# Performance work log

Hardware: AMD Instinct MI355X
Metric: run time of the kernel (lower is better)

## Reference

```python
import jax, jax.numpy as jnp
import numpy as np

NC = 8          # num_classes
NA = 5          # num_anchors
NOOBJ = 1.0     # noobject_scale
OBJ = 10.0      # object_scale
COORD = 1.0     # coord_scale
CLASS = 1.0     # class_scale
THRESH = 0.6    # sil_thresh
ANCHORS = np.array([1.08, 1.19, 3.42, 4.41, 6.63, 11.38, 9.42, 5.11, 16.62, 10.52], np.float32)


def _iou_xywh(px, py, pw, pl, gx, gy, gw, gl):
    # IoU of center-format boxes (matches bbox_ious with x1y1x2y2=False)
    mx = jnp.minimum(px - pw * 0.5, gx - gw * 0.5)
    Mx = jnp.maximum(px + pw * 0.5, gx + gw * 0.5)
    my = jnp.minimum(py - pl * 0.5, gy - gl * 0.5)
    My = jnp.maximum(py + pl * 0.5, gy + gl * 0.5)
    cw = pw + gw - (Mx - mx)
    ch = pl + gl - (My - my)
    inter = jnp.where((cw > 0) & (ch > 0), cw * ch, 0.0)
    return inter / (pw * pl + gw * gl - inter)


def setup_inputs() -> dict:
    key = jax.random.key(0)
    k1, k2, k3 = jax.random.split(key, 3)
    nB, nT, nH, nW = 16, 50, 96, 96
    output = jax.random.normal(k1, (nB, NA * (7 + NC), nH, nW), jnp.float32)
    t = jax.random.uniform(k2, (nB, nT, 7), jnp.float32)
    cls_col = jax.random.randint(k3, (nB, nT, 1), 0, NC).astype(jnp.float32)
    geom = t[..., 1:5] * 0.9 + 0.05            # x,y,w,l in (0,1), nonzero
    euler = t[..., 5:7] * 2.0 - 1.0            # im,re in [-1,1]
    target = jnp.concatenate([cls_col, geom, euler], axis=-1)
    return {"output": output, "target": target, "anchors": jnp.asarray(ANCHORS)}


def reference(output, target, anchors):
    sg = jax.lax.stop_gradient
    nB, _, nH, nW = output.shape
    nA, nC = NA, NC
    N = nB * nA * nH * nW

    out = output.reshape(nB, nA, 7 + nC, nH, nW)
    x = jax.nn.sigmoid(out[:, :, 0])
    y = jax.nn.sigmoid(out[:, :, 1])
    w = out[:, :, 2]
    l = out[:, :, 3]
    im = out[:, :, 4]
    re = out[:, :, 5]
    conf = jax.nn.sigmoid(out[:, :, 6])
    # [nB*nA, nC, nH*nW].transpose(1,2) -> flat [N, nC]
    cls_prob = out[:, :, 7:].transpose(0, 1, 3, 4, 2).reshape(N, nC)

    # ---- predicted boxes (detached, as in the torch .data path) ----
    anc = sg(anchors)
    aw = anc[0::2]
    ah = anc[1::2]
    grid_x = jnp.arange(nW, dtype=jnp.float32)[None, None, None, :]
    grid_y = jnp.arange(nH, dtype=jnp.float32)[None, None, :, None]
    px = sg(x) + grid_x
    py = sg(y) + grid_y
    pw = jnp.exp(sg(w)) * aw[None, :, None, None]
    pl = jnp.exp(sg(l)) * ah[None, :, None, None]

    # ---- build_targets (vectorized) ----
    tgt = sg(target)
    nT = tgt.shape[1]
    # break-at-first-zero semantics of the original loop
    valid = jnp.cumprod((tgt[:, :, 1] != 0).astype(jnp.int32), axis=1).astype(bool)  # [nB,nT]
    gx = tgt[:, :, 1] * nW
    gy = tgt[:, :, 2] * nH
    gw = tgt[:, :, 3] * nW
    gl = tgt[:, :, 4] * nH

    # pairwise IoU pred-vs-GT: [nB, nT, nA, nH, nW]
    ious = _iou_xywh(px[:, None], py[:, None], pw[:, None], pl[:, None],
                     gx[:, :, None, None, None], gy[:, :, None, None, None],
                     gw[:, :, None, None, None], gl[:, :, None, None, None])
    ious = jnp.where(valid[:, :, None, None, None], ious, 0.0)
    max_iou = ious.max(axis=1)                              # [nB,nA,nH,nW]
    conf_mask = jnp.where(max_iou > THRESH, 0.0, NOOBJ)

    # best anchor per GT: IoU of (0,0,gw,gl) vs (0,0,aw,ah)
    inter = jnp.minimum(gw[..., None], aw) * jnp.minimum(gl[..., None], ah)
    anc_iou = inter / (gw[..., None] * gl[..., None] + aw * ah - inter)    # [nB,nT,nA]
    best_n = jnp.argmax(anc_iou, axis=-1)                   # first max, like strict '>' scan

    gi = jnp.clip(gx.astype(jnp.int32), 0, nW - 1)
    gj = jnp.clip(gy.astype(jnp.int32), 0, nH - 1)
    b_idx = jnp.arange(nB)[:, None]
    idx = ((b_idx * nA + best_n) * nH + gj) * nW + gi       # [nB,nT] flat cell index
    idx_safe = jnp.minimum(idx, N - 1)
    idx_sc = jnp.where(valid, idx, N).ravel()               # OOB -> dropped by scatter

    def scat(vals):
        return jnp.zeros(N, jnp.float32).at[idx_sc].set(vals.ravel(), mode='drop').reshape(nB, nA, nH, nW)

    coord_mask = scat(jnp.ones_like(gx))
    cls_mask_f = coord_mask.reshape(N)
    conf_mask = conf_mask.reshape(N).at[idx_sc].set(jnp.full(nB * nT, OBJ), mode='drop').reshape(nB, nA, nH, nW)

    tx = scat(gx - gi)
    ty = scat(gy - gj)
    tw = scat(jnp.log(gw / aw[best_n]))
    tl = scat(jnp.log(gl / ah[best_n]))
    tim = scat(tgt[:, :, 5])
    tre = scat(tgt[:, :, 6])
    tcls_f = scat(tgt[:, :, 0]).reshape(N)

    # IoU of each GT with the predicted box at its assigned cell
    pb = jnp.stack([px, py, pw, pl], axis=-1).reshape(N, 4)
    pbg = pb[idx_safe]                                      # [nB,nT,4]
    iou_t = _iou_xywh(pbg[..., 0], pbg[..., 1], pbg[..., 2], pbg[..., 3], gx, gy, gw, gl)
    tconf = scat(iou_t)

    nGT = valid.sum()
    nCorrect = (valid & (iou_t > 0.5)).sum()

    # ---- losses ----
    def mse(a, t, m):
        return jnp.sum((a * m - t * m) ** 2)

    loss_x = COORD * mse(x, tx, coord_mask)
    loss_y = COORD * mse(y, ty, coord_mask)
    loss_w = COORD * mse(w, tw, coord_mask)
    loss_l = COORD * mse(l, tl, coord_mask)
    loss_conf = mse(conf, tconf, conf_mask)
    loss_im = COORD * mse(im, tim, coord_mask)
    loss_re = COORD * mse(re, tre, coord_mask)

    logp = jax.nn.log_softmax(cls_prob, axis=-1)
    tcls_idx = tcls_f.astype(jnp.int32)
    ce = -jnp.take_along_axis(logp, tcls_idx[:, None], axis=1)[:, 0]
    loss_cls = CLASS * jnp.sum(ce * cls_mask_f)

    loss = loss_x + loss_y + loss_w + loss_l + loss_conf + loss_cls + loss_im + loss_re
    return loss, nCorrect, nGT
```

## Files before the change

kernel.cpp:

```cpp
#include <hip/hip_runtime.h>
#include <math.h>

namespace {

constexpr int kB = 16, kT = 50, kH = 96, kW = 96, kA = 5;
constexpr int kCH = 15;
constexpr int kPlane = kH * kW;
constexpr int kCellsPerBlk = 1024;
constexpr int kBlkPerPlane = kPlane / kCellsPerBlk;
constexpr int kNoobjBlocks = kB * kA * kBlkPerPlane;
constexpr int kReducerBlk = kB + kNoobjBlocks;
constexpr float kObjSq = 100.0f;


__device__ __forceinline__ void publish(unsigned long long* slot, float v) {
  unsigned lo = __float_as_uint(v);
  unsigned long long pk = ((unsigned long long)(~lo) << 32) | lo;
  atomicExch(slot, pk);
}

__device__ __forceinline__ float fast_sigmoid(float v) {
  return __builtin_amdgcn_rcpf(1.0f + __expf(-v));
}

__device__ __forceinline__ void make_rec(
    const float* __restrict__ tgt, const float* __restrict__ anc, int b,
    int lane, float4& r, float& c, int& vidx, bool& valid, float& gx,
    float& gy, float& gw, float& gl, int& bn, int& gi, int& gj, float& c0,
    float& e5, float& e6) {
  const float* tp = tgt + (b * kT + (lane < kT ? lane : 0)) * 7;
  c0 = tp[0];
  const float g1 = tp[1], g2 = tp[2], g3 = tp[3], g4 = tp[4];
  e5 = tp[5];
  e6 = tp[6];
  unsigned long long nzm = __ballot((lane < kT) && (g1 != 0.0f));
  valid = false;
  vidx = -1;
  bn = 0; gi = 0; gj = 0;
  gx = g1 * kW; gy = g2 * kH; gw = g3 * kW; gl = g4 * kH;
  r = make_float4(1e30f, -1e30f, 1e30f, -1e30f);
  c = 1e30f;
  if (lane < kT) {
    valid = ((~nzm) & ((1ull << (lane + 1)) - 1ull)) == 0ull;
    float best = -1.0f;
    for (int a = 0; a < kA; ++a) {
      float aw = anc[2 * a], ah = anc[2 * a + 1];
      float inter = fminf(gw, aw) * fminf(gl, ah);
      float iou = inter / (gw * gl + aw * ah - inter);
      if (iou > best) { best = iou; bn = a; }
    }
    gi = min(max((int)gx, 0), kW - 1);
    gj = min(max((int)gy, 0), kH - 1);
    int idx = ((b * kA + bn) * kH + gj) * kW + gi;
    vidx = valid ? idx : -1;
    if (valid) {
      r = make_float4(gx - gw * 0.5f, gx + gw * 0.5f, gy - gl * 0.5f,
                      gy + gl * 0.5f);
      c = 0.375f * (gw * gl);
    }
  }
}

__global__ __launch_bounds__(256) void fused_kernel(
    const float* __restrict__ out, const float* __restrict__ tgt,
    const float* __restrict__ anc, unsigned long long* __restrict__ ws,
    float* __restrict__ d_out) {
  __shared__ float s_red[4];

  const int blk = blockIdx.x;
  const int tid = threadIdx.x;

  if (blk == kReducerBlk) {
    float L = 0.0f, C = 0.0f, G = 0.0f;
    for (int s = tid; s < 768; s += 256) {
      unsigned long long v;
      for (;;) {
        v = atomicAdd(&ws[s], 0ULL);
        if ((unsigned)(v >> 32) == (unsigned)(~(unsigned)v)) break;
        __builtin_amdgcn_s_sleep(2);
      }
      float f = __uint_as_float((unsigned)v);
      if (s < 736) L += f;
      else if (s < 752) C += f;
      else G += f;
    }
    for (int off = 32; off > 0; off >>= 1) {
      L += __shfl_down(L, off, 64);
      C += __shfl_down(C, off, 64);
      G += __shfl_down(G, off, 64);
    }
    __shared__ float sr[12];
    const int wv = tid >> 6;
    if ((tid & 63) == 0) { sr[wv] = L; sr[4 + wv] = C; sr[8 + wv] = G; }
    __syncthreads();
    if (tid == 0) {
      d_out[0] = sr[0] + sr[1] + sr[2] + sr[3];
      d_out[1] = sr[4] + sr[5] + sr[6] + sr[7];
      d_out[2] = sr[8] + sr[9] + sr[10] + sr[11];
    }
    return;
  }

  if (blk < kB) {
    if (tid >= 64) return;
    const int b = blk, t = tid;
    float4 r; float c; int vidx; bool valid;
    float gx, gy, gw, gl, c0, e5, e6; int bn, gi, gj;
    make_rec(tgt, anc, b, t, r, c, vidx, valid, gx, gy, gw, gl, bn, gi, gj,
             c0, e5, e6);
    const int ngt = __popcll(__ballot(valid));

    float loss = 0.0f;
    int ncorr = 0;
    if (valid) {
      bool owner = true;
      for (int t2 = 0; t2 < kT; ++t2) {
        int v2 = __shfl(vidx, t2);
        owner &= !((t2 > t) && (v2 == vidx));
      }
      const float* p =
          out + ((size_t)(b * kA + bn) * kCH) * kPlane + gj * kW + gi;
      const float xr = p[0], yr = p[kPlane];
      const float wr = p[2 * kPlane], lr = p[3 * kPlane];
      const float aw = anc[2 * bn], ah = anc[2 * bn + 1];
      const float x = 1.0f / (1.0f + expf(-xr));
      const float y = 1.0f / (1.0f + expf(-yr));
      const float px = x + (float)gi, py = y + (float)gj;
      const float pw = expf(wr) * aw, pl = expf(lr) * ah;
      float mx = fminf(px - pw * 0.5f, gx - gw * 0.5f);
      float Mx = fmaxf(px + pw * 0.5f, gx + gw * 0.5f);
      float my = fminf(py - pl * 0.5f, gy - gl * 0.5f);
      float My = fmaxf(py + pl * 0.5f, gy + gl * 0.5f);
      float cw = pw + gw - (Mx - mx);
      float ch = pl + gl - (My - my);
      float inter = (cw > 0.0f && ch > 0.0f) ? cw * ch : 0.0f;
      float iou = inter / (pw * pl + gw * gl - inter);
      ncorr = (iou > 0.5f) ? 1 : 0;

      if (owner) {
        const float imv = p[4 * kPlane], rev = p[5 * kPlane];
        const float cr = p[6 * kPlane];
        float tx = gx - (float)gi, ty = gy - (float)gj;
        float tw = logf(gw / aw), tl = logf(gl / ah);
        float conf = 1.0f / (1.0f + expf(-cr));
        float dx = x - tx, dy = y - ty, dw = wr - tw, dl = lr - tl;
        float di = imv - e5, dr = rev - e6, dc = conf - iou;
        loss = dx * dx + dy * dy + dw * dw + dl * dl + di * di + dr * dr +
               kObjSq * dc * dc;
        const float cc0 = p[7 * kPlane],  cc1 = p[8 * kPlane];
        const float cc2 = p[9 * kPlane],  cc3 = p[10 * kPlane];
        const float cc4 = p[11 * kPlane], cc5 = p[12 * kPlane];
        const float cc6 = p[13 * kPlane], cc7 = p[14 * kPlane];
        float m = fmaxf(fmaxf(fmaxf(cc0, cc1), fmaxf(cc2, cc3)),
                        fmaxf(fmaxf(cc4, cc5), fmaxf(cc6, cc7)));
        float s = expf(cc0 - m) + expf(cc1 - m) + expf(cc2 - m) +
                  expf(cc3 - m) + expf(cc4 - m) + expf(cc5 - m) +
                  expf(cc6 - m) + expf(cc7 - m);
        float lse = m + logf(s);
        int ci = min(max((int)c0, 0), 7);
        float csel = cc0;
        csel = (ci == 1) ? cc1 : csel;
        csel = (ci == 2) ? cc2 : csel;
        csel = (ci == 3) ? cc3 : csel;
        csel = (ci == 4) ? cc4 : csel;
        csel = (ci == 5) ? cc5 : csel;
        csel = (ci == 6) ? cc6 : csel;
        csel = (ci == 7) ? cc7 : csel;
        loss += lse - csel;

        float pxf = fast_sigmoid(xr) + (float)gi;
        float pyf = fast_sigmoid(yr) + (float)gj;
        float pwf = __expf(wr) * aw, plf = __expf(lr) * ah;
        float px0 = pxf - pwf * 0.5f, px1 = pxf + pwf * 0.5f;
        float py0 = pyf - plf * 0.5f, py1 = pyf + plf * 0.5f;
        float pthr = 0.375f * (pwf * plf);
        float conff = fast_sigmoid(cr);
        float hh = -1e30f;
        for (int t2 = 0; t2 < kT; ++t2) {
          float x0 = __shfl(r.x, t2), x1 = __shfl(r.y, t2);
          float y0 = __shfl(r.z, t2), y1 = __shfl(r.w, t2);
          float cc = __shfl(c, t2);
          float cw2 = fminf(px1, x1) - fmaxf(px0, x0);
          float ch2 = fminf(py1, y1) - fmaxf(py0, y0);
          float a2 = fmaxf(cw2, 0.0f);
          hh = fmaxf(hh, __builtin_fmaf(a2, ch2, -cc));
        }
        if (!(hh > pthr)) loss -= conff * conff;
      }
    }
    for (int off = 32; off > 0; off >>= 1) {
      loss += __shfl_down(loss, off, 64);
      ncorr += __shfl_down(ncorr, off, 64);
    }
    if (t == 0) {
      publish(&ws[kNoobjBlocks + b], loss);
      publish(&ws[kNoobjBlocks + kB + b], (float)ncorr);
      publish(&ws[kNoobjBlocks + 2 * kB + b], (float)ngt);
    }
    return;
  }

  const int nb = blk - kB;
  const int plane = nb / kBlkPerPlane;
  const int b = plane / kA, a = plane % kA;
  const int base = (nb % kBlkPerPlane) * kCellsPerBlk;

  float4 r; float c; int vidx; bool valid;
  float gx, gy, gw, gl, c0, e5, e6; int bn, gi, gj;
  make_rec(tgt, anc, b, tid & 63, r, c, vidx, valid, gx, gy, gw, gl, bn, gi,
           gj, c0, e5, e6);

  const int cell0 = base + 4 * tid;
  const int j = cell0 / kW;
  const int i0 = cell0 - j * kW;

  const float* pb = out + ((size_t)plane * kCH) * kPlane + cell0;
  const float4 xv = *(const float4*)(pb);
  const float4 yv = *(const float4*)(pb + kPlane);
  const float4 wv = *(const float4*)(pb + 2 * kPlane);
  const float4 lv = *(const float4*)(pb + 3 * kPlane);
  const float4 cv = *(const float4*)(pb + 6 * kPlane);
  const float aw = anc[2 * a], ah = anc[2 * a + 1];

  const float xs[4] = {xv.x, xv.y, xv.z, xv.w};
  const float ys[4] = {yv.x, yv.y, yv.z, yv.w};
  const float wss[4] = {wv.x, wv.y, wv.z, wv.w};
  const float ls[4] = {lv.x, lv.y, lv.z, lv.w};
  const float crs[4] = {cv.x, cv.y, cv.z, cv.w};

  float px0[4], px1[4], py0[4], py1[4], pthr[4], conf[4], hh[4];
#pragma unroll
  for (int e = 0; e < 4; ++e) {
    float px = fast_sigmoid(xs[e]) + (float)(i0 + e);
    float py = fast_sigmoid(ys[e]) + (float)j;
    float pw = __expf(wss[e]) * aw;
    float pl = __expf(ls[e]) * ah;
    px0[e] = px - pw * 0.5f; px1[e] = px + pw * 0.5f;
    py0[e] = py - pl * 0.5f; py1[e] = py + pl * 0.5f;
    pthr[e] = 0.375f * (pw * pl);
    conf[e] = fast_sigmoid(crs[e]);
    hh[e] = -1e30f;
  }

#pragma unroll
  for (int t = 0; t < kT; ++t) {
    const float x0 = __shfl(r.x, t), x1 = __shfl(r.y, t);
    const float y0 = __shfl(r.z, t), y1 = __shfl(r.w, t);
    const float cc = __shfl(c, t);
#pragma unroll
    for (int e = 0; e < 4; ++e) {
      float cw = fminf(px1[e], x1) - fmaxf(px0[e], x0);
      float ch = fminf(py1[e], y1) - fmaxf(py0[e], y0);
      float a2 = fmaxf(cw, 0.0f);
      hh[e] = fmaxf(hh[e], __builtin_fmaf(a2, ch, -cc));
    }
  }

  float loss = 0.0f;
#pragma unroll
  for (int e = 0; e < 4; ++e)
    loss += (hh[e] > pthr[e]) ? 0.0f : conf[e] * conf[e];

  for (int off = 32; off > 0; off >>= 1) loss += __shfl_down(loss, off, 64);
  if ((tid & 63) == 0) s_red[tid >> 6] = loss;
  __syncthreads();
  if (tid == 0)
    publish(&ws[nb], s_red[0] + s_red[1] + s_red[2] + s_red[3]);
}

}

extern "C" void kernel_launch(void* const* d_in, const int* in_sizes, int n_in,
                              void* d_out, int out_size, void* d_ws,
                              size_t ws_size, hipStream_t stream) {
  const float* output = (const float*)d_in[0];
  const float* target = (const float*)d_in[1];
  const float* anchors = (const float*)d_in[2];
  float* outp = (float*)d_out;
  unsigned long long* ws = (unsigned long long*)d_ws;

  fused_kernel<<<kReducerBlk + 1, 256, 0, stream>>>(output, target, anchors,
                                                    ws, outp);
}
```

Baseline: 17.30 us.

## Compute noobj IoU threshold test in packed fp16 with two cells per thread

Replaces the fp32 per-cell IoU-versus-threshold loop over ground-truth boxes with packed half2 min/max/fma arithmetic, so each thread handles two cells per instruction. Cells per thread drop from four to two, which doubles the block count, and reducer slot bounds are now derived from constants. The packed math roughly halves ALU work in the inner loop but loses fp16 precision in the threshold comparison. That could flip borderline noobj decisions, and coordinates up to about 96 squared approach fp16 limits.

```diff
diff --git a/kernel.cpp b/kernel.cpp
--- a/kernel.cpp
+++ b/kernel.cpp
@@ -6,11 +6,15 @@
 constexpr int kB = 16, kT = 50, kH = 96, kW = 96, kA = 5;
 constexpr int kCH = 15;
 constexpr int kPlane = kH * kW;
-constexpr int kCellsPerBlk = 1024;
+constexpr int kCellsPerThread = 2;
+constexpr int kCellsPerBlk = 256 * kCellsPerThread;
 constexpr int kBlkPerPlane = kPlane / kCellsPerBlk;
 constexpr int kNoobjBlocks = kB * kA * kBlkPerPlane;
 constexpr int kReducerBlk = kB + kNoobjBlocks;
+constexpr int kSlots = kNoobjBlocks + 3 * kB;
 constexpr float kObjSq = 100.0f;
+
+typedef _Float16 h2 __attribute__((ext_vector_type(2)));
 
 
 __device__ __forceinline__ void publish(unsigned long long* slot, float v) {
@@ -23,11 +27,23 @@
   return __builtin_amdgcn_rcpf(1.0f + __expf(-v));
 }
 
+__device__ __forceinline__ h2 i2h(int v) {
+  union { int i; h2 h; } u; u.i = v; return u.h;
+}
+__device__ __forceinline__ int h2i(h2 h) {
+  union { int i; h2 h2v; } u; u.h2v = h; return u.i;
+}
+__device__ __forceinline__ h2 mk_h2(float a, float b) {
+  h2 r; r.x = (_Float16)a; r.y = (_Float16)b; return r;
+}
+
+struct PkRec { int x0, x1, y0, y1, nc; };
+
 __device__ __forceinline__ void make_rec(
     const float* __restrict__ tgt, const float* __restrict__ anc, int b,
-    int lane, float4& r, float& c, int& vidx, bool& valid, float& gx,
-    float& gy, float& gw, float& gl, int& bn, int& gi, int& gj, float& c0,
-    float& e5, float& e6) {
+    int lane, PkRec& pk, int& vidx, bool& valid, float& gx, float& gy,
+    float& gw, float& gl, int& bn, int& gi, int& gj, float& c0, float& e5,
+    float& e6) {
   const float* tp = tgt + (b * kT + (lane < kT ? lane : 0)) * 7;
   c0 = tp[0];
   const float g1 = tp[1], g2 = tp[2], g3 = tp[3], g4 = tp[4];
@@ -38,8 +54,11 @@
   vidx = -1;
   bn = 0; gi = 0; gj = 0;
   gx = g1 * kW; gy = g2 * kH; gw = g3 * kW; gl = g4 * kH;
-  r = make_float4(1e30f, -1e30f, 1e30f, -1e30f);
-  c = 1e30f;
+  pk.x0 = h2i(mk_h2(30000.f, 30000.f));
+  pk.x1 = h2i(mk_h2(-30000.f, -30000.f));
+  pk.y0 = h2i(mk_h2(30000.f, 30000.f));
+  pk.y1 = h2i(mk_h2(-30000.f, -30000.f));
+  pk.nc = h2i(mk_h2(-30000.f, -30000.f));
   if (lane < kT) {
     valid = ((~nzm) & ((1ull << (lane + 1)) - 1ull)) == 0ull;
     float best = -1.0f;
@@ -54,11 +73,37 @@
     int idx = ((b * kA + bn) * kH + gj) * kW + gi;
     vidx = valid ? idx : -1;
     if (valid) {
-      r = make_float4(gx - gw * 0.5f, gx + gw * 0.5f, gy - gl * 0.5f,
-                      gy + gl * 0.5f);
-      c = 0.375f * (gw * gl);
-    }
-  }
+      float x0 = gx - gw * 0.5f, x1 = gx + gw * 0.5f;
+      float y0 = gy - gl * 0.5f, y1 = gy + gl * 0.5f;
+      float c = 0.375f * (gw * gl);
+      pk.x0 = h2i(mk_h2(x0, x0));
+      pk.x1 = h2i(mk_h2(x1, x1));
+      pk.y0 = h2i(mk_h2(y0, y0));
+      pk.y1 = h2i(mk_h2(y1, y1));
+      pk.nc = h2i(mk_h2(-c, -c));
+    }
+  }
+}
+
+__device__ __forceinline__ h2 hit_margin(const PkRec& pk, h2 px0, h2 px1,
+                                         h2 py0, h2 py1) {
+  h2 hh = mk_h2(-60000.f, -60000.f);
+  const h2 zero = mk_h2(0.f, 0.f);
+#pragma unroll
+  for (int t = 0; t < kT; ++t) {
+    const h2 X0 = i2h(__shfl(pk.x0, t, 64));
+    const h2 X1 = i2h(__shfl(pk.x1, t, 64));
+    const h2 Y0 = i2h(__shfl(pk.y0, t, 64));
+    const h2 Y1 = i2h(__shfl(pk.y1, t, 64));
+    const h2 NC = i2h(__shfl(pk.nc, t, 64));
+    h2 cw = __builtin_elementwise_min(px1, X1) -
+            __builtin_elementwise_max(px0, X0);
+    h2 ch = __builtin_elementwise_min(py1, Y1) -
+            __builtin_elementwise_max(py0, Y0);
+    h2 aa = __builtin_elementwise_max(cw, zero);
+    hh = __builtin_elementwise_max(hh, __builtin_elementwise_fma(aa, ch, NC));
+  }
+  return hh;
 }
 
 __global__ __launch_bounds__(256) void fused_kernel(
@@ -72,7 +117,7 @@
 
   if (blk == kReducerBlk) {
     float L = 0.0f, C = 0.0f, G = 0.0f;
-    for (int s = tid; s < 768; s += 256) {
+    for (int s = tid; s < kSlots; s += 256) {
       unsigned long long v;
       for (;;) {
         v = atomicAdd(&ws[s], 0ULL);
@@ -80,8 +125,8 @@
         __builtin_amdgcn_s_sleep(2);
       }
       float f = __uint_as_float((unsigned)v);
-      if (s < 736) L += f;
-      else if (s < 752) C += f;
+      if (s < kNoobjBlocks + kB) L += f;
+      else if (s < kNoobjBlocks + 2 * kB) C += f;
       else G += f;
     }
     for (int off = 32; off > 0; off >>= 1) {
@@ -104,9 +149,9 @@
   if (blk < kB) {
     if (tid >= 64) return;
     const int b = blk, t = tid;
-    float4 r; float c; int vidx; bool valid;
+    PkRec pk; int vidx; bool valid;
     float gx, gy, gw, gl, c0, e5, e6; int bn, gi, gj;
-    make_rec(tgt, anc, b, t, r, c, vidx, valid, gx, gy, gw, gl, bn, gi, gj,
+    make_rec(tgt, anc, b, t, pk, vidx, valid, gx, gy, gw, gl, bn, gi, gj,
              c0, e5, e6);
     const int ngt = __popcll(__ballot(valid));
 
@@ -171,21 +216,15 @@
         float pxf = fast_sigmoid(xr) + (float)gi;
         float pyf = fast_sigmoid(yr) + (float)gj;
         float pwf = __expf(wr) * aw, plf = __expf(lr) * ah;
-        float px0 = pxf - pwf * 0.5f, px1 = pxf + pwf * 0.5f;
-        float py0 = pyf - plf * 0.5f, py1 = pyf + plf * 0.5f;
-        float pthr = 0.375f * (pwf * plf);
+        float px0f = pxf - pwf * 0.5f, px1f = pxf + pwf * 0.5f;
+        float py0f = pyf - plf * 0.5f, py1f = pyf + plf * 0.5f;
+        float pthrf = 0.375f * (pwf * plf);
         float conff = fast_sigmoid(cr);
-        float hh = -1e30f;
-        for (int t2 = 0; t2 < kT; ++t2) {
-          float x0 = __shfl(r.x, t2), x1 = __shfl(r.y, t2);
-          float y0 = __shfl(r.z, t2), y1 = __shfl(r.w, t2);
-          float cc = __shfl(c, t2);
-          float cw2 = fminf(px1, x1) - fmaxf(px0, x0);
-          float ch2 = fminf(py1, y1) - fmaxf(py0, y0);
-          float a2 = fmaxf(cw2, 0.0f);
-          hh = fmaxf(hh, __builtin_fmaf(a2, ch2, -cc));
-        }
-        if (!(hh > pthr)) loss -= conff * conff;
+        h2 hh = hit_margin(pk, mk_h2(px0f, px0f), mk_h2(px1f, px1f),
+                           mk_h2(py0f, py0f), mk_h2(py1f, py1f));
+        float hh0 = (float)hh.x;
+        float pt0 = (float)(_Float16)pthrf;
+        if (!(hh0 > pt0)) loss -= conff * conff;
       }
     }
     for (int off = 32; off > 0; off >>= 1) {
@@ -205,61 +244,53 @@
   const int b = plane / kA, a = plane % kA;
   const int base = (nb % kBlkPerPlane) * kCellsPerBlk;
 
-  float4 r; float c; int vidx; bool valid;
+  PkRec pk; int vidx; bool valid;
   float gx, gy, gw, gl, c0, e5, e6; int bn, gi, gj;
-  make_rec(tgt, anc, b, tid & 63, r, c, vidx, valid, gx, gy, gw, gl, bn, gi,
+  make_rec(tgt, anc, b, tid & 63, pk, vidx, valid, gx, gy, gw, gl, bn, gi,
            gj, c0, e5, e6);
 
-  const int cell0 = base + 4 * tid;
+  const int cell0 = base + 2 * tid;
   const int j = cell0 / kW;
   const int i0 = cell0 - j * kW;
 
   const float* pb = out + ((size_t)plane * kCH) * kPlane + cell0;
-  const float4 xv = *(const float4*)(pb);
-  const float4 yv = *(const float4*)(pb + kPlane);
-  const float4 wv = *(const float4*)(pb + 2 * kPlane);
-  const float4 lv = *(const float4*)(pb + 3 * kPlane);
-  const float4 cv = *(const float4*)(pb + 6 * kPlane);
+  const float2 xv = *(const float2*)(pb);
+  const float2 yv = *(const float2*)(pb + kPlane);
+  const float2 wv = *(const float2*)(pb + 2 * kPlane);
+  const float2 lv = *(const float2*)(pb + 3 * kPlane);
+  const float2 cv = *(const float2*)(pb + 6 * kPlane);
   const float aw = anc[2 * a], ah = anc[2 * a + 1];
 
-  const float xs[4] = {xv.x, xv.y, xv.z, xv.w};
-  const float ys[4] = {yv.x, yv.y, yv.z, yv.w};
-  const float wss[4] = {wv.x, wv.y, wv.z, wv.w};
-  const float ls[4] = {lv.x, lv.y, lv.z, lv.w};
-  const float crs[4] = {cv.x, cv.y, cv.z, cv.w};
-
-  float px0[4], px1[4], py0[4], py1[4], pthr[4], conf[4], hh[4];
+  float px0f[2], px1f[2], py0f[2], py1f[2], pthrf[2], conf[2];
+  const float xs[2] = {xv.x, xv.y};
+  const float ys[2] = {yv.x, yv.y};
+  const float wss[2] = {wv.x, wv.y};
+  const float ls[2] = {lv.x, lv.y};
+  const float crs[2] = {cv.x, cv.y};
 #pragma unroll
-  for (int e = 0; e < 4; ++e) {
+  for (int e = 0; e < 2; ++e) {
     float px = fast_sigmoid(xs[e]) + (float)(i0 + e);
     float py = fast_sigmoid(ys[e]) + (float)j;
     float pw = __expf(wss[e]) * aw;
     float pl = __expf(ls[e]) * ah;
-    px0[e] = px - pw * 0.5f; px1[e] = px + pw * 0.5f;
-    py0[e] = py - pl * 0.5f; py1[e] = py + pl * 0.5f;
-    pthr[e] = 0.375f * (pw * pl);
+    px0f[e] = px - pw * 0.5f; px1f[e] = px + pw * 0.5f;
+    py0f[e] = py - pl * 0.5f; py1f[e] = py + pl * 0.5f;
+    pthrf[e] = 0.375f * (pw * pl);
     conf[e] = fast_sigmoid(crs[e]);
-    hh[e] = -1e30f;
-  }
-
-#pragma unroll
-  for (int t = 0; t < kT; ++t) {
-    const float x0 = __shfl(r.x, t), x1 = __shfl(r.y, t);
-    const float y0 = __shfl(r.z, t), y1 = __shfl(r.w, t);
-    const float cc = __shfl(c, t);
-#pragma unroll
-    for (int e = 0; e < 4; ++e) {
-      float cw = fminf(px1[e], x1) - fmaxf(px0[e], x0);
-      float ch = fminf(py1[e], y1) - fmaxf(py0[e], y0);
-      float a2 = fmaxf(cw, 0.0f);
-      hh[e] = fmaxf(hh[e], __builtin_fmaf(a2, ch, -cc));
-    }
-  }
+  }
+
+  h2 hh = hit_margin(pk, mk_h2(px0f[0], px0f[1]), mk_h2(px1f[0], px1f[1]),
+                     mk_h2(py0f[0], py0f[1]), mk_h2(py1f[0], py1f[1]));
 
   float loss = 0.0f;
-#pragma unroll
-  for (int e = 0; e < 4; ++e)
-    loss += (hh[e] > pthr[e]) ? 0.0f : conf[e] * conf[e];
+  {
+    float hh0 = (float)hh.x;
+    float hh1 = (float)hh.y;
+    float pt0 = (float)(_Float16)pthrf[0];
+    float pt1 = (float)(_Float16)pthrf[1];
+    loss += (hh0 > pt0) ? 0.0f : conf[0] * conf[0];
+    loss += (hh1 > pt1) ? 0.0f : conf[1] * conf[1];
+  }
 
   for (int off = 32; off > 0; off >>= 1) loss += __shfl_down(loss, off, 64);
   if ((tid & 63) == 0) s_red[tid >> 6] = loss;
```

After: 23.90 us. 1.38x slower.

## Publish per-wave partials and poll reducer slots in batched non-blocking loop

Applied to the files above, without the earlier changes.

Each wave of the no-object blocks now publishes its own partial sum to a separate workspace slot, which removes the shared-memory reduction and the block barrier. The reducer block polls all of its slots in one batched pass per iteration instead of spinning on each slot in turn. The target-record setup is also moved after the feature loads so the two can overlap. The cost is four times more slots for the reducer to read and more atomic polling traffic.

```diff
diff --git a/kernel.cpp b/kernel.cpp
--- a/kernel.cpp
+++ b/kernel.cpp
@@ -10,6 +10,9 @@
 constexpr int kBlkPerPlane = kPlane / kCellsPerBlk;
 constexpr int kNoobjBlocks = kB * kA * kBlkPerPlane;
 constexpr int kReducerBlk = kB + kNoobjBlocks;
+constexpr int kNoobjSlots = kNoobjBlocks * 4;
+constexpr int kSlots = kNoobjSlots + 3 * kB;
+constexpr int kPer = (kSlots + 255) / 256;
 constexpr float kObjSq = 100.0f;
 
 
@@ -65,24 +68,39 @@
     const float* __restrict__ out, const float* __restrict__ tgt,
     const float* __restrict__ anc, unsigned long long* __restrict__ ws,
     float* __restrict__ d_out) {
-  __shared__ float s_red[4];
-
   const int blk = blockIdx.x;
   const int tid = threadIdx.x;
 
   if (blk == kReducerBlk) {
     float L = 0.0f, C = 0.0f, G = 0.0f;
-    for (int s = tid; s < 768; s += 256) {
-      unsigned long long v;
-      for (;;) {
-        v = atomicAdd(&ws[s], 0ULL);
-        if ((unsigned)(v >> 32) == (unsigned)(~(unsigned)v)) break;
-        __builtin_amdgcn_s_sleep(2);
+    unsigned long long vv[kPer];
+    bool got[kPer];
+    int left = 0;
+#pragma unroll
+    for (int q = 0; q < kPer; ++q) {
+      got[q] = (tid + q * 256) >= kSlots;
+      left += got[q] ? 0 : 1;
+    }
+    while (left > 0) {
+#pragma unroll
+      for (int q = 0; q < kPer; ++q)
+        if (!got[q]) vv[q] = atomicAdd(&ws[tid + q * 256], 0ULL);
+#pragma unroll
+      for (int q = 0; q < kPer; ++q) {
+        if (!got[q]) {
+          unsigned long long v = vv[q];
+          if ((unsigned)(v >> 32) == (unsigned)(~(unsigned)v)) {
+            got[q] = true;
+            --left;
+            float f = __uint_as_float((unsigned)v);
+            const int s = tid + q * 256;
+            if (s < kNoobjSlots + kB) L += f;
+            else if (s < kNoobjSlots + 2 * kB) C += f;
+            else G += f;
+          }
+        }
       }
-      float f = __uint_as_float((unsigned)v);
-      if (s < 736) L += f;
-      else if (s < 752) C += f;
-      else G += f;
+      if (left) __builtin_amdgcn_s_sleep(2);
     }
     for (int off = 32; off > 0; off >>= 1) {
       L += __shfl_down(L, off, 64);
@@ -193,9 +211,9 @@
       ncorr += __shfl_down(ncorr, off, 64);
     }
     if (t == 0) {
-      publish(&ws[kNoobjBlocks + b], loss);
-      publish(&ws[kNoobjBlocks + kB + b], (float)ncorr);
-      publish(&ws[kNoobjBlocks + 2 * kB + b], (float)ngt);
+      publish(&ws[kNoobjSlots + b], loss);
+      publish(&ws[kNoobjSlots + kB + b], (float)ncorr);
+      publish(&ws[kNoobjSlots + 2 * kB + b], (float)ngt);
     }
     return;
   }
@@ -204,11 +222,7 @@
   const int plane = nb / kBlkPerPlane;
   const int b = plane / kA, a = plane % kA;
   const int base = (nb % kBlkPerPlane) * kCellsPerBlk;
-
-  float4 r; float c; int vidx; bool valid;
-  float gx, gy, gw, gl, c0, e5, e6; int bn, gi, gj;
-  make_rec(tgt, anc, b, tid & 63, r, c, vidx, valid, gx, gy, gw, gl, bn, gi,
-           gj, c0, e5, e6);
+  const int lane = tid & 63, wid = tid >> 6;
 
   const int cell0 = base + 4 * tid;
   const int j = cell0 / kW;
@@ -221,6 +235,11 @@
   const float4 lv = *(const float4*)(pb + 3 * kPlane);
   const float4 cv = *(const float4*)(pb + 6 * kPlane);
   const float aw = anc[2 * a], ah = anc[2 * a + 1];
+
+  float4 r; float c; int vidx; bool valid;
+  float gx, gy, gw, gl, c0, e5, e6; int bn, gi, gj;
+  make_rec(tgt, anc, b, lane, r, c, vidx, valid, gx, gy, gw, gl, bn, gi, gj,
+           c0, e5, e6);
 
   const float xs[4] = {xv.x, xv.y, xv.z, xv.w};
   const float ys[4] = {yv.x, yv.y, yv.z, yv.w};
@@ -262,10 +281,7 @@
     loss += (hh[e] > pthr[e]) ? 0.0f : conf[e] * conf[e];
 
   for (int off = 32; off > 0; off >>= 1) loss += __shfl_down(loss, off, 64);
-  if ((tid & 63) == 0) s_red[tid >> 6] = loss;
-  __syncthreads();
-  if (tid == 0)
-    publish(&ws[nb], s_red[0] + s_red[1] + s_red[2] + s_red[3]);
+  if (lane == 0) publish(&ws[nb * 4 + wid], loss);
 }
 
 }
```

After: 17.50 us. Within noise of the previous version (+1.1%).
